# Performance work log

Hardware: AMD Instinct MI355X
Metric: run time of the kernel (lower is better)

Reference implementation:

```python
import jax, jax.numpy as jnp
import numpy as np

D_MODEL = 1024
N_HEADS = 16
HEAD_DIM = D_MODEL // N_HEADS
D_FF = 4096
RANK = 8
B, T = 4, 2048


def _layernorm(x, g, b, eps=1e-5):
    mu = jnp.mean(x, axis=-1, keepdims=True)
    var = jnp.var(x, axis=-1, keepdims=True)
    return (x - mu) * jax.lax.rsqrt(var + eps) * g + b


def _dyn_linear(x, W, A, b_dyn, bias=None):
    # base: x [b,t,i] @ W.T  (W is [o,i] like nn.Linear)
    out = jnp.einsum('bti,oi->bto', x, W)
    if bias is not None:
        out = out + bias
    # per-sample low-rank delta: (x @ b_dyn.T) @ A.T
    delta = jnp.einsum('bti,bri,or->bto', x, b_dyn, A)
    return out + delta


def setup_inputs() -> dict:
    key = jax.random.key(0)
    ks = jax.random.split(key, 24)
    s = 0.02
    inp = {
        'x': jax.random.normal(ks[0], (B, T, D_MODEL), jnp.float32),
        'dyn_q': jax.random.normal(ks[1], (B, RANK, D_MODEL), jnp.float32) * s,
        'dyn_k': jax.random.normal(ks[2], (B, RANK, D_MODEL), jnp.float32) * s,
        'dyn_v': jax.random.normal(ks[3], (B, RANK, D_MODEL), jnp.float32) * s,
        'dyn_ff1': jax.random.normal(ks[4], (B, RANK, D_MODEL), jnp.float32) * s,
        'dyn_ff2': jax.random.normal(ks[5], (B, RANK, D_FF), jnp.float32) * s,
        'Wq': jax.random.normal(ks[6], (D_MODEL, D_MODEL), jnp.float32) / np.sqrt(D_MODEL),
        'Aq': jax.random.normal(ks[7], (D_MODEL, RANK), jnp.float32) * s,
        'Wk': jax.random.normal(ks[8], (D_MODEL, D_MODEL), jnp.float32) / np.sqrt(D_MODEL),
        'Ak': jax.random.normal(ks[9], (D_MODEL, RANK), jnp.float32) * s,
        'Wv': jax.random.normal(ks[10], (D_MODEL, D_MODEL), jnp.float32) / np.sqrt(D_MODEL),
        'Av': jax.random.normal(ks[11], (D_MODEL, RANK), jnp.float32) * s,
        'Wo': jax.random.normal(ks[12], (D_MODEL, D_MODEL), jnp.float32) / np.sqrt(D_MODEL),
        'W1': jax.random.normal(ks[13], (D_FF, D_MODEL), jnp.float32) / np.sqrt(D_MODEL),
        'b1': jnp.zeros((D_FF,), jnp.float32),
        'A1': jax.random.normal(ks[14], (D_FF, RANK), jnp.float32) * s,
        'W2': jax.random.normal(ks[15], (D_MODEL, D_FF), jnp.float32) / np.sqrt(D_FF),
        'b2': jnp.zeros((D_MODEL,), jnp.float32),
        'A2': jax.random.normal(ks[16], (D_MODEL, RANK), jnp.float32) * s,
        'g1': jnp.ones((D_MODEL,), jnp.float32),
        'beta1': jnp.zeros((D_MODEL,), jnp.float32),
        'g2': jnp.ones((D_MODEL,), jnp.float32),
        'beta2': jnp.zeros((D_MODEL,), jnp.float32),
    }
    return inp


def reference(x, dyn_q, dyn_k, dyn_v, dyn_ff1, dyn_ff2,
              Wq, Aq, Wk, Ak, Wv, Av, Wo,
              W1, b1, A1, W2, b2, A2,
              g1, beta1, g2, beta2):
    bsz, seq_len, _ = x.shape
    residual = x
    h = _layernorm(x, g1, beta1)
    q = _dyn_linear(h, Wq, Aq, dyn_q)
    k = _dyn_linear(h, Wk, Ak, dyn_k)
    v = _dyn_linear(h, Wv, Av, dyn_v)
    # [b, t, h, d] -> [b, h, t, d]
    q = q.reshape(bsz, seq_len, N_HEADS, HEAD_DIM).transpose(0, 2, 1, 3)
    k = k.reshape(bsz, seq_len, N_HEADS, HEAD_DIM).transpose(0, 2, 1, 3)
    v = v.reshape(bsz, seq_len, N_HEADS, HEAD_DIM).transpose(0, 2, 1, 3)
    score = jnp.einsum('bhqd,bhkd->bhqk', q, k) / np.sqrt(HEAD_DIM).astype(np.float32)
    attn = jax.nn.softmax(score, axis=-1)
    ctx = jnp.einsum('bhqk,bhkd->bhqd', attn, v)
    ctx = ctx.transpose(0, 2, 1, 3).reshape(bsz, seq_len, D_MODEL)
    x = residual + jnp.einsum('bti,oi->bto', ctx, Wo)  # dropout p=0
    residual = x
    h = _layernorm(x, g2, beta2)
    ff = jax.nn.gelu(_dyn_linear(h, W1, A1, dyn_ff1, bias=b1), approximate=False)
    ff = _dyn_linear(ff, W2, A2, dyn_ff2, bias=b2)
    return residual + ff
```

## Files before the change

### kernel.cpp

```cpp
#include <hip/hip_runtime.h>
#include <math.h>

#define D_MODEL 1024
#define D_FF    4096
#define RANK    8
#define BATCH   4
#define SEQ     2048
#define MTOT    (BATCH*SEQ)
#define NHEADS  16
#define HDIM    64

typedef __attribute__((ext_vector_type(8))) __bf16 bf16x8;
typedef __attribute__((ext_vector_type(4))) float f32x4;
typedef __attribute__((ext_vector_type(8))) unsigned short u16x8;
typedef __attribute__((ext_vector_type(4))) unsigned short u16x4;

__device__ __forceinline__ unsigned short f2bf(float f) {
  __bf16 h = (__bf16)f;
  return __builtin_bit_cast(unsigned short, h);
}
__device__ __forceinline__ float bf2f(unsigned short h) {
  union { unsigned int u; float f; } v; v.u = ((unsigned int)h) << 16;
  return v.f;
}

__device__ __forceinline__ f32x4 mfma16(bf16x8 a, bf16x8 b, f32x4 c) {
  return __builtin_amdgcn_mfma_f32_16x16x32_bf16(a, b, c, 0, 0, 0);
}

#define GLDS(g, l) __builtin_amdgcn_global_load_lds( \
    (const __attribute__((address_space(1))) void*)(g), \
    (__attribute__((address_space(3))) void*)(l), 16, 0, 0)

__global__ __launch_bounds__(256) void cvt_bf16_all(
    const float* __restrict__ s0, const float* __restrict__ s1,
    const float* __restrict__ s2, const float* __restrict__ s3,
    const float* __restrict__ s4, const float* __restrict__ s5,
    unsigned short* __restrict__ d0, unsigned short* __restrict__ d1,
    unsigned short* __restrict__ d2, unsigned short* __restrict__ d3,
    unsigned short* __restrict__ d4, unsigned short* __restrict__ d5)
{
  const int b = blockIdx.x;
  const float* src; unsigned short* dst; int base;
  if (b < 512)       { src = s0; dst = d0; base = b; }
  else if (b < 1024) { src = s1; dst = d1; base = b - 512; }
  else if (b < 1536) { src = s2; dst = d2; base = b - 1024; }
  else if (b < 2048) { src = s3; dst = d3; base = b - 1536; }
  else if (b < 4096) { src = s4; dst = d4; base = b - 2048; }
  else               { src = s5; dst = d5; base = b - 4096; }
  const size_t i = (size_t)base * 256 + threadIdx.x;
  const float4 a  = *reinterpret_cast<const float4*>(src + i * 8);
  const float4 c  = *reinterpret_cast<const float4*>(src + i * 8 + 4);
  u16x8 o;
  o[0] = f2bf(a.x); o[1] = f2bf(a.y); o[2] = f2bf(a.z); o[3] = f2bf(a.w);
  o[4] = f2bf(c.x); o[5] = f2bf(c.y); o[6] = f2bf(c.z); o[7] = f2bf(c.w);
  *reinterpret_cast<u16x8*>(dst + i * 8) = o;
}

__global__ __launch_bounds__(256) void ln_fwd(const float* __restrict__ x,
                                              const float* __restrict__ g,
                                              const float* __restrict__ be,
                                              unsigned short* __restrict__ out)
{
  const int row = blockIdx.x;
  const int t = threadIdx.x;
  const float* xr = x + (size_t)row * D_MODEL;
  float4 vv = *reinterpret_cast<const float4*>(xr + t * 4);
  float s  = vv.x + vv.y + vv.z + vv.w;
  float s2 = vv.x * vv.x + vv.y * vv.y + vv.z * vv.z + vv.w * vv.w;
#pragma unroll
  for (int mm = 1; mm < 64; mm <<= 1) { s += __shfl_xor(s, mm); s2 += __shfl_xor(s2, mm); }
  __shared__ float red[8];
  const int w = t >> 6, l = t & 63;
  if (l == 0) { red[w] = s; red[4 + w] = s2; }
  __syncthreads();
  s  = red[0] + red[1] + red[2] + red[3];
  s2 = red[4] + red[5] + red[6] + red[7];
  float mean = s * (1.f / D_MODEL);
  float var  = s2 * (1.f / D_MODEL) - mean * mean;
  float rstd = rsqrtf(var + 1e-5f);
  float4 gv = *reinterpret_cast<const float4*>(g  + t * 4);
  float4 bv = *reinterpret_cast<const float4*>(be + t * 4);
  u16x4 o;
  o[0] = f2bf((vv.x - mean) * rstd * gv.x + bv.x);
  o[1] = f2bf((vv.y - mean) * rstd * gv.y + bv.y);
  o[2] = f2bf((vv.z - mean) * rstd * gv.z + bv.z);
  o[3] = f2bf((vv.w - mean) * rstd * gv.w + bv.w);
  *reinterpret_cast<u16x4*>(out + (size_t)row * D_MODEL + t * 4) = o;
}

template<int ILEN>
__global__ __launch_bounds__(256) void dyn_u(const unsigned short* __restrict__ hmat,
                                             const float* __restrict__ dyn,
                                             float* __restrict__ u)
{
  const int tid = threadIdx.x, w = tid >> 6, l = tid & 63;
  const int m0 = blockIdx.x * 16 + w * 4;
  const int b = m0 / SEQ;
  const float* dynb = dyn + (size_t)b * RANK * ILEN;
  float acc[4][RANK] = {};
  for (int s = 0; s < ILEN / 64; ++s) {
    const int i = l + s * 64;
    float hv[4];
#pragma unroll
    for (int rr = 0; rr < 4; ++rr) hv[rr] = bf2f(hmat[(size_t)(m0 + rr) * ILEN + i]);
#pragma unroll
    for (int r = 0; r < RANK; ++r) {
      float d = dynb[(size_t)r * ILEN + i];
#pragma unroll
      for (int rr = 0; rr < 4; ++rr) acc[rr][r] += hv[rr] * d;
    }
  }
#pragma unroll
  for (int rr = 0; rr < 4; ++rr)
#pragma unroll
    for (int r = 0; r < RANK; ++r) {
      float a = acc[rr][r];
#pragma unroll
      for (int mm = 1; mm < 64; mm <<= 1) a += __shfl_xor(a, mm);
      if (l == 0) u[(size_t)(m0 + rr) * RANK + r] = a;
    }
}

__global__ __launch_bounds__(256) void dyn_u_qkv(const unsigned short* __restrict__ hmat,
                                                 const float* __restrict__ dq,
                                                 const float* __restrict__ dk,
                                                 const float* __restrict__ dv,
                                                 float* __restrict__ u)
{
  const int tid = threadIdx.x, w = tid >> 6, l = tid & 63;
  const int m0 = blockIdx.x * 16 + w * 4;
  const int b = m0 / SEQ;
  const float* db0 = dq + (size_t)b * RANK * D_MODEL;
  const float* db1 = dk + (size_t)b * RANK * D_MODEL;
  const float* db2 = dv + (size_t)b * RANK * D_MODEL;
  float acc[4][3 * RANK] = {};
  for (int s = 0; s < D_MODEL / 64; ++s) {
    const int i = l + s * 64;
    float hv[4];
#pragma unroll
    for (int rr = 0; rr < 4; ++rr) hv[rr] = bf2f(hmat[(size_t)(m0 + rr) * D_MODEL + i]);
#pragma unroll
    for (int r = 0; r < RANK; ++r) {
      float d0 = db0[(size_t)r * D_MODEL + i];
      float d1 = db1[(size_t)r * D_MODEL + i];
      float d2 = db2[(size_t)r * D_MODEL + i];
#pragma unroll
      for (int rr = 0; rr < 4; ++rr) {
        acc[rr][r] += hv[rr] * d0;
        acc[rr][RANK + r] += hv[rr] * d1;
        acc[rr][2 * RANK + r] += hv[rr] * d2;
      }
    }
  }
#pragma unroll
  for (int g = 0; g < 3; ++g)
#pragma unroll
    for (int rr = 0; rr < 4; ++rr)
#pragma unroll
      for (int r = 0; r < RANK; ++r) {
        float a = acc[rr][g * RANK + r];
#pragma unroll
        for (int mm = 1; mm < 64; mm <<= 1) a += __shfl_xor(a, mm);
        if (l == 0) u[((size_t)g * MTOT + m0 + rr) * RANK + r] = a;
      }
}

template<int NDIM, int KDIM, int MODE, int BN>
__global__ __launch_bounds__(512, (BN == 256) ? 1 : 2)
void gemm_bt(const unsigned short* __restrict__ A,
             const unsigned short* __restrict__ B,
             void* __restrict__ outp,
             void* __restrict__ outp2,
             const float* __restrict__ uvec,
             const float* __restrict__ Ad0,
             const float* __restrict__ Ad1,
             const float* __restrict__ Ad2,
             const float* __restrict__ bias,
             const float* __restrict__ resid)
{
  constexpr bool HAS_DYN = (MODE == 2 || MODE == 3 || MODE == 5);
  constexpr int WN = BN / 64;
  constexpr int WM = 8 / WN;
  constexpr int MSPAN = 256 / WM;
  constexpr int NI = MSPAN / 16;
  __shared__ unsigned short sAB[2][(256 + BN) * 64];
  const int tid = threadIdx.x;
  const int w = tid >> 6, l = tid & 63;

  constexpr int NBX = NDIM / BN;
  constexpr int NWG = NBX * (MTOT / 256);
  const int bid = blockIdx.y * NBX + blockIdx.x;
  const int sbid = (bid & 7) * (NWG / 8) + (bid >> 3);
  const int tm = (sbid / NBX) * 256, tn = (sbid % NBX) * BN;
  const int wm = w / WN, wn = w % WN;

  f32x4 acc[NI][4] = {};

  const int srow = l >> 3;
  const int sc8 = (l & 7) ^ (srow & 7);
  const unsigned short* Ag = A + (size_t)(tm + srow) * KDIM + sc8 * 8;
  const unsigned short* Bg = B + (size_t)(tn + srow) * KDIM + sc8 * 8;

  const int arow = wm * MSPAN + (l & 15);
  const int bcol = wn * 64 + (l & 15);
  const int kb0 = l >> 4;
  const int swz = l & 7;

  constexpr int NT = KDIM / 64;

  auto stage = [&](int buf, int kt) {
    unsigned short* bA = &sAB[buf][0];
    unsigned short* bB = &sAB[buf][256 * 64];
#pragma unroll
    for (int it = 0; it < 4; ++it) {
      const int st = w * 4 + it;
      GLDS(Ag + (size_t)(st * 8) * KDIM + kt, bA + st * 512);
    }
#pragma unroll
    for (int it = 0; it < WN; ++it) {
      const int st = w * WN + it;
      GLDS(Bg + (size_t)(st * 8) * KDIM + kt, bB + st * 512);
    }
  };

  stage(0, 0);
  asm volatile("s_waitcnt vmcnt(0)" ::: "memory");
  __syncthreads();

  int cur = 0;
  for (int t = 0; t < NT; ++t) {
    if (t + 1 < NT) stage(cur ^ 1, (t + 1) * 64);

    const unsigned short* sA_ = &sAB[cur][0];
    const unsigned short* sB_ = &sAB[cur][256 * 64];
#pragma unroll
    for (int kk = 0; kk < 2; ++kk) {
      bf16x8 af[NI], bfv[4];
      const int kphys = ((kk * 4 + kb0) ^ swz) << 3;
#pragma unroll
      for (int i = 0; i < NI; ++i)
        af[i] = *reinterpret_cast<const bf16x8*>(&sA_[(arow + i * 16) * 64 + kphys]);
#pragma unroll
      for (int j = 0; j < 4; ++j)
        bfv[j] = *reinterpret_cast<const bf16x8*>(&sB_[(bcol + j * 16) * 64 + kphys]);
#pragma unroll
      for (int i = 0; i < NI; ++i)
#pragma unroll
        for (int j = 0; j < 4; ++j)
          acc[i][j] = mfma16(af[i], bfv[j], acc[i][j]);
    }
    __syncthreads();
    cur ^= 1;
  }

  const int rbase = tm + wm * MSPAN + ((l >> 4) << 2);
  const int cbase = tn + wn * 64 + (l & 15);

  const int seg = tn >> 10;
  const float* Ad = Ad0;
  const float* uv = uvec;
  if constexpr (MODE == 5) {
    Ad = (seg == 0) ? Ad0 : (seg == 1) ? Ad1 : Ad2;
    uv = uvec + (size_t)seg * ((size_t)MTOT * RANK);
  }

#pragma unroll
  for (int i = 0; i < NI; ++i) {
    float uu[4][8];
    if constexpr (HAS_DYN) {
#pragma unroll
      for (int r = 0; r < 4; ++r) {
        const float* up = uv + (size_t)(rbase + i * 16 + r) * RANK;
#pragma unroll
        for (int p = 0; p < 8; ++p) uu[r][p] = up[p];
      }
    }
#pragma unroll
    for (int j = 0; j < 4; ++j) {
      const int col = cbase + j * 16;
      float ad[8];
      if constexpr (HAS_DYN) {
#pragma unroll
        for (int p = 0; p < 8; ++p) ad[p] = Ad[(size_t)col * RANK + p];
      }
      float vv4[4];
#pragma unroll
      for (int r = 0; r < 4; ++r) {
        const int row = rbase + i * 16 + r;
        float v = acc[i][j][r];
        if constexpr (HAS_DYN) {
#pragma unroll
          for (int p = 0; p < 8; ++p) v += uu[r][p] * ad[p];
        }
        if constexpr (MODE == 2) {
          v += bias[col];
          v = 0.5f * v * (1.f + erff(v * 0.70710678118654752f));
        }
        if constexpr (MODE == 1) {
          v += resid[(size_t)row * NDIM + col];
        }
        if constexpr (MODE == 3) {
          v += bias[col] + resid[(size_t)row * NDIM + col];
        }
        if constexpr (MODE == 5) {
          if (seg == 0) v *= 0.18033688011112042f;
        }
        vv4[r] = v;
      }
      if constexpr (MODE == 2) {
#pragma unroll
        for (int r = 0; r < 4; ++r)
          ((unsigned short*)outp)[(size_t)(rbase + i * 16 + r) * NDIM + col] = f2bf(vv4[r]);
      } else if constexpr (MODE == 5) {
        const int cl = col & 1023;
        if (seg < 2) {
#pragma unroll
          for (int r = 0; r < 4; ++r)
            ((unsigned short*)outp)[((size_t)seg * MTOT + rbase + i * 16 + r) * D_MODEL + cl] =
                f2bf(vv4[r]);
        } else {
          const int row0 = rbase + i * 16;
          const int bb = row0 >> 11, t0 = row0 & (SEQ - 1);
          const int hh = cl >> 6, dd = cl & 63;
          const int jj = (t0 >> 4) & 3;
          unsigned short* vb = &((unsigned short*)outp2)[
              (((size_t)bb * NHEADS + hh) * HDIM + dd) * SEQ + (t0 & ~63)];
#pragma unroll
          for (int dlt = 0; dlt < 4; ++dlt)
            vb[((t0 & 15) + dlt) * 4 + jj] = f2bf(vv4[dlt]);
        }
      } else {
#pragma unroll
        for (int r = 0; r < 4; ++r)
          ((float*)outp)[(size_t)(rbase + i * 16 + r) * NDIM + col] = vv4[r];
      }
    }
  }
}

__global__ __launch_bounds__(256, 4) void attn_fwd(const unsigned short* __restrict__ q,
                                                   const unsigned short* __restrict__ k,
                                                   const unsigned short* __restrict__ vt,
                                                   unsigned short* __restrict__ ctx)
{
  __shared__ unsigned short sK[64 * 64];
  __shared__ unsigned short sV[64 * 64];
  __shared__ unsigned short sP[4][32 * 64];

  const int tid = threadIdx.x, w = tid >> 6, l = tid & 63;
  const int lin = blockIdx.y * (SEQ / 128) + blockIdx.x;
  const int W = (lin & 7) * ((BATCH * NHEADS * SEQ / 128) / 8) + (lin >> 3);
  const int bh = W >> 4, b = bh >> 4, hh = bh & 15;
  const int q0 = (W & 15) * 128 + w * 32;
  const size_t base = ((size_t)b * SEQ) * D_MODEL + hh * HDIM;
  const size_t vtbase = (size_t)bh * HDIM * SEQ;

  bf16x8 qf[2][2];
#pragma unroll
  for (int i = 0; i < 2; ++i)
#pragma unroll
    for (int ks = 0; ks < 2; ++ks)
      qf[i][ks] = *reinterpret_cast<const bf16x8*>(
          &q[base + (size_t)(q0 + i * 16 + (l & 15)) * D_MODEL + ks * 32 + (l >> 4) * 8]);

  bf16x8 ones;
#pragma unroll
  for (int e = 0; e < 8; ++e) ones[e] = (__bf16)1.0f;

  f32x4 oacc[2][4] = {};
  f32x4 sumacc[2] = {};

  const int srow8 = l >> 3;
  const int sswz = (l & 7) ^ (srow8 & 7);
  const unsigned short* kg = k + base + (size_t)srow8 * D_MODEL + sswz * 8;
  const unsigned short* vg = vt + vtbase + (size_t)srow8 * SEQ + sswz * 8;

  const int kb0 = l >> 4;
  const int c15 = l & 15;

  for (int kt = 0; kt < SEQ; kt += 64) {
    __syncthreads();
#pragma unroll
    for (int it = 0; it < 2; ++it) {
      const int c = it * 4 + w;
      GLDS(kg + (size_t)(kt + c * 8) * D_MODEL, sK + c * 512);
      GLDS(vg + (size_t)(c * 8) * SEQ + kt, sV + c * 512);
    }
    asm volatile("s_waitcnt vmcnt(0)" ::: "memory");
    __syncthreads();

    f32x4 sacc[2][4] = {};
    __builtin_amdgcn_s_setprio(1);
#pragma unroll
    for (int ks = 0; ks < 2; ++ks) {
#pragma unroll
      for (int j = 0; j < 4; ++j) {
        const int row = j * 16 + (l & 15);
        bf16x8 kf = *reinterpret_cast<const bf16x8*>(
            &sK[row * 64 + (((ks * 4 + kb0) ^ (row & 7)) << 3)]);
#pragma unroll
        for (int i = 0; i < 2; ++i) sacc[i][j] = mfma16(qf[i][ks], kf, sacc[i][j]);
      }
    }
    __builtin_amdgcn_s_setprio(0);

#pragma unroll
    for (int i = 0; i < 2; ++i) {
#pragma unroll
      for (int r = 0; r < 4; ++r) {
        float p[4];
#pragma unroll
        for (int j = 0; j < 4; ++j) p[j] = __builtin_exp2f(sacc[i][j][r]);
        const int prow = i * 16 + ((l >> 4) << 2) + r;
        u16x4 pk;
        pk[0] = f2bf(p[0]); pk[1] = f2bf(p[1]); pk[2] = f2bf(p[2]); pk[3] = f2bf(p[3]);
        *reinterpret_cast<u16x4*>(
            &sP[w][prow * 64 + ((((c15 >> 1) ^ (prow & 7)) << 3) | ((c15 & 1) << 2))]) = pk;
      }
    }

    __builtin_amdgcn_s_setprio(1);
#pragma unroll
    for (int ks = 0; ks < 2; ++ks) {
      bf16x8 pf[2];
#pragma unroll
      for (int i = 0; i < 2; ++i) {
        const int prw = i * 16 + (l & 15);
        pf[i] = *reinterpret_cast<const bf16x8*>(
            &sP[w][prw * 64 + (((ks * 4 + kb0) ^ (prw & 7)) << 3)]);
      }
#pragma unroll
      for (int j = 0; j < 4; ++j) {
        const int row = j * 16 + (l & 15);
        bf16x8 vf = *reinterpret_cast<const bf16x8*>(
            &sV[row * 64 + (((ks * 4 + kb0) ^ (row & 7)) << 3)]);
#pragma unroll
        for (int i = 0; i < 2; ++i) oacc[i][j] = mfma16(pf[i], vf, oacc[i][j]);
      }
#pragma unroll
      for (int i = 0; i < 2; ++i) sumacc[i] = mfma16(pf[i], ones, sumacc[i]);
    }
    __builtin_amdgcn_s_setprio(0);
  }

#pragma unroll
  for (int i = 0; i < 2; ++i)
#pragma unroll
    for (int r = 0; r < 4; ++r) {
      float inv = 1.f / sumacc[i][r];
      int row = q0 + i * 16 + ((l >> 4) << 2) + r;
#pragma unroll
      for (int j = 0; j < 4; ++j)
        ctx[base + (size_t)row * D_MODEL + j * 16 + (l & 15)] = f2bf(oacc[i][j][r] * inv);
    }
}

extern "C" void kernel_launch(void* const* d_in, const int* in_sizes, int n_in,
                              void* d_out, int out_size, void* d_ws, size_t ws_size,
                              hipStream_t stream)
{
  (void)in_sizes; (void)n_in; (void)out_size; (void)ws_size;
  const float* x      = (const float*)d_in[0];
  const float* dyn_q  = (const float*)d_in[1];
  const float* dyn_k  = (const float*)d_in[2];
  const float* dyn_v  = (const float*)d_in[3];
  const float* dyn_f1 = (const float*)d_in[4];
  const float* dyn_f2 = (const float*)d_in[5];
  const float* Wq = (const float*)d_in[6];
  const float* Aq = (const float*)d_in[7];
  const float* Wk = (const float*)d_in[8];
  const float* Ak = (const float*)d_in[9];
  const float* Wv = (const float*)d_in[10];
  const float* Av = (const float*)d_in[11];
  const float* Wo = (const float*)d_in[12];
  const float* W1 = (const float*)d_in[13];
  const float* b1 = (const float*)d_in[14];
  const float* A1 = (const float*)d_in[15];
  const float* W2 = (const float*)d_in[16];
  const float* b2 = (const float*)d_in[17];
  const float* A2 = (const float*)d_in[18];
  const float* g1 = (const float*)d_in[19];
  const float* be1 = (const float*)d_in[20];
  const float* g2 = (const float*)d_in[21];
  const float* be2 = (const float*)d_in[22];

  char* ws = (char*)d_ws;
  size_t o = 0;
  auto take = [&](size_t b) { size_t r = o; o += (b + 255) & ~(size_t)255; return r; };
  const size_t o_wq = take((size_t)D_MODEL * D_MODEL * 2);
  const size_t o_wk = take((size_t)D_MODEL * D_MODEL * 2);
  const size_t o_wv = take((size_t)D_MODEL * D_MODEL * 2);
  const size_t o_wo = take((size_t)D_MODEL * D_MODEL * 2);
  const size_t o_w1 = take((size_t)D_FF * D_MODEL * 2);
  const size_t o_w2 = take((size_t)D_FF * D_MODEL * 2);
  const size_t o_h1 = take((size_t)MTOT * D_MODEL * 2);
  const size_t o_q  = take((size_t)MTOT * D_MODEL * 2);
  const size_t o_k  = take((size_t)MTOT * D_MODEL * 2);
  const size_t o_v  = take((size_t)MTOT * D_MODEL * 2);
  const size_t o_u  = take((size_t)MTOT * RANK * 4 * 3);
  const size_t o_ff = take((size_t)MTOT * D_FF * 2);

  unsigned short* wq_b = (unsigned short*)(ws + o_wq);
  unsigned short* wk_b = (unsigned short*)(ws + o_wk);
  unsigned short* wv_b = (unsigned short*)(ws + o_wv);
  unsigned short* wo_b = (unsigned short*)(ws + o_wo);
  unsigned short* w1_b = (unsigned short*)(ws + o_w1);
  unsigned short* w2_b = (unsigned short*)(ws + o_w2);
  unsigned short* h1   = (unsigned short*)(ws + o_h1);
  unsigned short* qb   = (unsigned short*)(ws + o_q);
  unsigned short* vtb  = (unsigned short*)(ws + o_v);
  float* u_q  = (float*)(ws + o_u);
  float* u_k  = u_q + (size_t)MTOT * RANK;
  unsigned short* ctx = h1;
  float* x2 = (float*)(ws + o_q);
  unsigned short* h2 = vtb;
  float* u_f1 = u_q;
  float* u_f2 = u_k;
  unsigned short* ffb = (unsigned short*)(ws + o_ff);

  cvt_bf16_all<<<6144, 256, 0, stream>>>(Wq, Wk, Wv, Wo, W1, W2,
                                         wq_b, wk_b, wv_b, wo_b, w1_b, w2_b);

  ln_fwd<<<MTOT, 256, 0, stream>>>(x, g1, be1, h1);

  dyn_u_qkv<<<MTOT / 16, 256, 0, stream>>>(h1, dyn_q, dyn_k, dyn_v, u_q);

  gemm_bt<3 * D_MODEL, D_MODEL, 5, 256><<<dim3(3 * D_MODEL / 256, MTOT / 256), 512, 0, stream>>>(
      h1, wq_b, qb, vtb, u_q, Aq, Ak, Av, nullptr, nullptr);

  attn_fwd<<<dim3(SEQ / 128, BATCH * NHEADS), 256, 0, stream>>>(
      qb, qb + (size_t)MTOT * D_MODEL, vtb, ctx);

  gemm_bt<D_MODEL, D_MODEL, 1, 128><<<dim3(D_MODEL / 128, MTOT / 256), 512, 0, stream>>>(
      ctx, wo_b, x2, nullptr, nullptr, nullptr, nullptr, nullptr, nullptr, x);

  ln_fwd<<<MTOT, 256, 0, stream>>>(x2, g2, be2, h2);

  dyn_u<D_MODEL><<<MTOT / 16, 256, 0, stream>>>(h2, dyn_f1, u_f1);
  gemm_bt<D_FF, D_MODEL, 2, 256><<<dim3(D_FF / 256, MTOT / 256), 512, 0, stream>>>(
      h2, w1_b, ffb, nullptr, u_f1, A1, nullptr, nullptr, b1, nullptr);

  dyn_u<D_FF><<<MTOT / 16, 256, 0, stream>>>(ffb, dyn_f2, u_f2);
  gemm_bt<D_MODEL, D_FF, 3, 128><<<dim3(D_MODEL / 128, MTOT / 256), 512, 0, stream>>>(
      ffb, w2_b, (float*)d_out, nullptr, u_f2, A2, nullptr, nullptr, b2, x2);
}
```

Measured before the change: 540.3 us.

## Fold low-rank dyn delta into GEMM as extra zero-padded K tile

Stores the per-row low-rank projections u and the A adapter matrices as bf16, zero-padded to a 64-wide K slab, and appends that slab as one extra K iteration of the MFMA GEMM main loop. This replaces the scalar 8-term FMA epilogue, with its per-element global loads of u and A, by a single extra matrix-core tile. It adds a small conversion kernel and rounds u and A to bf16, which slightly reduces precision of the delta term.

```diff
diff --git a/kernel.cpp b/kernel.cpp
--- a/kernel.cpp
+++ b/kernel.cpp
@@ -55,6 +55,34 @@
   o[0] = f2bf(a.x); o[1] = f2bf(a.y); o[2] = f2bf(a.z); o[3] = f2bf(a.w);
   o[4] = f2bf(c.x); o[5] = f2bf(c.y); o[6] = f2bf(c.z); o[7] = f2bf(c.w);
   *reinterpret_cast<u16x8*>(dst + i * 8) = o;
+}
+
+__global__ __launch_bounds__(256) void ad_ext(
+    const float* __restrict__ Aq, const float* __restrict__ Ak,
+    const float* __restrict__ Av, const float* __restrict__ A1,
+    const float* __restrict__ A2,
+    unsigned short* __restrict__ eqkv, unsigned short* __restrict__ e1,
+    unsigned short* __restrict__ e2)
+{
+  const int n = blockIdx.x * 256 + threadIdx.x;
+  const float* src; unsigned short* dst;
+  if (n < 3072) {
+    src = (n < 1024) ? (Aq + (size_t)n * 8)
+        : (n < 2048) ? (Ak + (size_t)(n - 1024) * 8)
+                     : (Av + (size_t)(n - 2048) * 8);
+    dst = eqkv + (size_t)n * 64;
+  } else if (n < 7168) {
+    src = A1 + (size_t)(n - 3072) * 8; dst = e1 + (size_t)(n - 3072) * 64;
+  } else {
+    src = A2 + (size_t)(n - 7168) * 8; dst = e2 + (size_t)(n - 7168) * 64;
+  }
+  u16x8 v;
+#pragma unroll
+  for (int p = 0; p < 8; ++p) v[p] = f2bf(src[p]);
+  *reinterpret_cast<u16x8*>(dst) = v;
+  u16x8 z = {};
+#pragma unroll
+  for (int c = 1; c < 8; ++c) *reinterpret_cast<u16x8*>(dst + c * 8) = z;
 }
 
 __global__ __launch_bounds__(256) void ln_fwd(const float* __restrict__ x,
@@ -92,7 +120,7 @@
 template<int ILEN>
 __global__ __launch_bounds__(256) void dyn_u(const unsigned short* __restrict__ hmat,
                                              const float* __restrict__ dyn,
-                                             float* __restrict__ u)
+                                             unsigned short* __restrict__ uext)
 {
   const int tid = threadIdx.x, w = tid >> 6, l = tid & 63;
   const int m0 = blockIdx.x * 16 + w * 4;
@@ -112,21 +140,27 @@
     }
   }
 #pragma unroll
-  for (int rr = 0; rr < 4; ++rr)
+  for (int rr = 0; rr < 4; ++rr) {
+    float red[RANK];
 #pragma unroll
     for (int r = 0; r < RANK; ++r) {
       float a = acc[rr][r];
 #pragma unroll
       for (int mm = 1; mm < 64; mm <<= 1) a += __shfl_xor(a, mm);
-      if (l == 0) u[(size_t)(m0 + rr) * RANK + r] = a;
-    }
+      red[r] = a;
+    }
+    const float mine =
+        (l == 0) ? red[0] : (l == 1) ? red[1] : (l == 2) ? red[2] : (l == 3) ? red[3] :
+        (l == 4) ? red[4] : (l == 5) ? red[5] : (l == 6) ? red[6] : (l == 7) ? red[7] : 0.f;
+    uext[(size_t)(m0 + rr) * 64 + l] = f2bf(mine);
+  }
 }
 
 __global__ __launch_bounds__(256) void dyn_u_qkv(const unsigned short* __restrict__ hmat,
                                                  const float* __restrict__ dq,
                                                  const float* __restrict__ dk,
                                                  const float* __restrict__ dv,
-                                                 float* __restrict__ u)
+                                                 unsigned short* __restrict__ uext)
 {
   const int tid = threadIdx.x, w = tid >> 6, l = tid & 63;
   const int m0 = blockIdx.x * 16 + w * 4;
@@ -156,14 +190,20 @@
 #pragma unroll
   for (int g = 0; g < 3; ++g)
 #pragma unroll
-    for (int rr = 0; rr < 4; ++rr)
+    for (int rr = 0; rr < 4; ++rr) {
+      float red[RANK];
 #pragma unroll
       for (int r = 0; r < RANK; ++r) {
         float a = acc[rr][g * RANK + r];
 #pragma unroll
         for (int mm = 1; mm < 64; mm <<= 1) a += __shfl_xor(a, mm);
-        if (l == 0) u[((size_t)g * MTOT + m0 + rr) * RANK + r] = a;
-      }
+        red[r] = a;
+      }
+      const float mine =
+          (l == 0) ? red[0] : (l == 1) ? red[1] : (l == 2) ? red[2] : (l == 3) ? red[3] :
+          (l == 4) ? red[4] : (l == 5) ? red[5] : (l == 6) ? red[6] : (l == 7) ? red[7] : 0.f;
+      uext[((size_t)g * MTOT + m0 + rr) * 64 + l] = f2bf(mine);
+    }
 }
 
 template<int NDIM, int KDIM, int MODE, int BN>
@@ -172,14 +212,12 @@
              const unsigned short* __restrict__ B,
              void* __restrict__ outp,
              void* __restrict__ outp2,
-             const float* __restrict__ uvec,
-             const float* __restrict__ Ad0,
-             const float* __restrict__ Ad1,
-             const float* __restrict__ Ad2,
+             const unsigned short* __restrict__ Aext,
+             const unsigned short* __restrict__ Bext,
              const float* __restrict__ bias,
              const float* __restrict__ resid)
 {
-  constexpr bool HAS_DYN = (MODE == 2 || MODE == 3 || MODE == 5);
+  constexpr bool HAS_EXT = (MODE == 2 || MODE == 3 || MODE == 5);
   constexpr int WN = BN / 64;
   constexpr int WM = 8 / WN;
   constexpr int MSPAN = 256 / WM;
@@ -194,6 +232,7 @@
   const int sbid = (bid & 7) * (NWG / 8) + (bid >> 3);
   const int tm = (sbid / NBX) * 256, tn = (sbid % NBX) * BN;
   const int wm = w / WN, wn = w % WN;
+  const int seg = tn >> 10;
 
   f32x4 acc[NI][4] = {};
 
@@ -201,6 +240,11 @@
   const int sc8 = (l & 7) ^ (srow & 7);
   const unsigned short* Ag = A + (size_t)(tm + srow) * KDIM + sc8 * 8;
   const unsigned short* Bg = B + (size_t)(tn + srow) * KDIM + sc8 * 8;
+  const size_t aeoff = (MODE == 5) ? (size_t)seg * MTOT : 0;
+  const unsigned short* Ae = HAS_EXT ?
+      (Aext + (aeoff + tm + srow) * 64 + sc8 * 8) : nullptr;
+  const unsigned short* Be = HAS_EXT ?
+      (Bext + (size_t)(tn + srow) * 64 + sc8 * 8) : nullptr;
 
   const int arow = wm * MSPAN + (l & 15);
   const int bcol = wn * 64 + (l & 15);
@@ -208,6 +252,7 @@
   const int swz = l & 7;
 
   constexpr int NT = KDIM / 64;
+  constexpr int TT = HAS_EXT ? NT + 1 : NT;
 
   auto stage = [&](int buf, int kt) {
     unsigned short* bA = &sAB[buf][0];
@@ -223,14 +268,30 @@
       GLDS(Bg + (size_t)(st * 8) * KDIM + kt, bB + st * 512);
     }
   };
+  auto stage_ext = [&](int buf) {
+    unsigned short* bA = &sAB[buf][0];
+    unsigned short* bB = &sAB[buf][256 * 64];
+#pragma unroll
+    for (int it = 0; it < 4; ++it) {
+      const int st = w * 4 + it;
+      GLDS(Ae + (size_t)(st * 8) * 64, bA + st * 512);
+    }
+#pragma unroll
+    for (int it = 0; it < WN; ++it) {
+      const int st = w * WN + it;
+      GLDS(Be + (size_t)(st * 8) * 64, bB + st * 512);
+    }
+  };
 
   stage(0, 0);
   asm volatile("s_waitcnt vmcnt(0)" ::: "memory");
   __syncthreads();
 
   int cur = 0;
-  for (int t = 0; t < NT; ++t) {
-    if (t + 1 < NT) stage(cur ^ 1, (t + 1) * 64);
+  for (int t = 0; t < TT; ++t) {
+    const int nt = t + 1;
+    if (nt < NT) stage(cur ^ 1, nt * 64);
+    else if (HAS_EXT && nt == NT) stage_ext(cur ^ 1);
 
     const unsigned short* sA_ = &sAB[cur][0];
     const unsigned short* sB_ = &sAB[cur][256 * 64];
@@ -257,42 +318,16 @@
   const int rbase = tm + wm * MSPAN + ((l >> 4) << 2);
   const int cbase = tn + wn * 64 + (l & 15);
 
-  const int seg = tn >> 10;
-  const float* Ad = Ad0;
-  const float* uv = uvec;
-  if constexpr (MODE == 5) {
-    Ad = (seg == 0) ? Ad0 : (seg == 1) ? Ad1 : Ad2;
-    uv = uvec + (size_t)seg * ((size_t)MTOT * RANK);
-  }
-
 #pragma unroll
   for (int i = 0; i < NI; ++i) {
-    float uu[4][8];
-    if constexpr (HAS_DYN) {
-#pragma unroll
-      for (int r = 0; r < 4; ++r) {
-        const float* up = uv + (size_t)(rbase + i * 16 + r) * RANK;
-#pragma unroll
-        for (int p = 0; p < 8; ++p) uu[r][p] = up[p];
-      }
-    }
 #pragma unroll
     for (int j = 0; j < 4; ++j) {
       const int col = cbase + j * 16;
-      float ad[8];
-      if constexpr (HAS_DYN) {
-#pragma unroll
-        for (int p = 0; p < 8; ++p) ad[p] = Ad[(size_t)col * RANK + p];
-      }
       float vv4[4];
 #pragma unroll
       for (int r = 0; r < 4; ++r) {
         const int row = rbase + i * 16 + r;
         float v = acc[i][j][r];
-        if constexpr (HAS_DYN) {
-#pragma unroll
-          for (int p = 0; p < 8; ++p) v += uu[r][p] * ad[p];
-        }
         if constexpr (MODE == 2) {
           v += bias[col];
           v = 0.5f * v * (1.f + erff(v * 0.70710678118654752f));
@@ -498,7 +533,10 @@
   const size_t o_q  = take((size_t)MTOT * D_MODEL * 2);
   const size_t o_k  = take((size_t)MTOT * D_MODEL * 2);
   const size_t o_v  = take((size_t)MTOT * D_MODEL * 2);
-  const size_t o_u  = take((size_t)MTOT * RANK * 4 * 3);
+  const size_t o_ue = take((size_t)3 * MTOT * 64 * 2);
+  const size_t o_aq = take((size_t)3 * D_MODEL * 64 * 2);
+  const size_t o_a1 = take((size_t)D_FF * 64 * 2);
+  const size_t o_a2 = take((size_t)D_MODEL * 64 * 2);
   const size_t o_ff = take((size_t)MTOT * D_FF * 2);
 
   unsigned short* wq_b = (unsigned short*)(ws + o_wq);
@@ -510,38 +548,41 @@
   unsigned short* h1   = (unsigned short*)(ws + o_h1);
   unsigned short* qb   = (unsigned short*)(ws + o_q);
   unsigned short* vtb  = (unsigned short*)(ws + o_v);
-  float* u_q  = (float*)(ws + o_u);
-  float* u_k  = u_q + (size_t)MTOT * RANK;
+  unsigned short* ueq  = (unsigned short*)(ws + o_ue);
+  unsigned short* uef1 = ueq;
+  unsigned short* uef2 = ueq + (size_t)MTOT * 64;
+  unsigned short* adeq = (unsigned short*)(ws + o_aq);
+  unsigned short* ade1 = (unsigned short*)(ws + o_a1);
+  unsigned short* ade2 = (unsigned short*)(ws + o_a2);
   unsigned short* ctx = h1;
   float* x2 = (float*)(ws + o_q);
   unsigned short* h2 = vtb;
-  float* u_f1 = u_q;
-  float* u_f2 = u_k;
   unsigned short* ffb = (unsigned short*)(ws + o_ff);
 
   cvt_bf16_all<<<6144, 256, 0, stream>>>(Wq, Wk, Wv, Wo, W1, W2,
                                          wq_b, wk_b, wv_b, wo_b, w1_b, w2_b);
+  ad_ext<<<32, 256, 0, stream>>>(Aq, Ak, Av, A1, A2, adeq, ade1, ade2);
 
   ln_fwd<<<MTOT, 256, 0, stream>>>(x, g1, be1, h1);
 
-  dyn_u_qkv<<<MTOT / 16, 256, 0, stream>>>(h1, dyn_q, dyn_k, dyn_v, u_q);
+  dyn_u_qkv<<<MTOT / 16, 256, 0, stream>>>(h1, dyn_q, dyn_k, dyn_v, ueq);
 
   gemm_bt<3 * D_MODEL, D_MODEL, 5, 256><<<dim3(3 * D_MODEL / 256, MTOT / 256), 512, 0, stream>>>(
-      h1, wq_b, qb, vtb, u_q, Aq, Ak, Av, nullptr, nullptr);
+      h1, wq_b, qb, vtb, ueq, adeq, nullptr, nullptr);
 
   attn_fwd<<<dim3(SEQ / 128, BATCH * NHEADS), 256, 0, stream>>>(
       qb, qb + (size_t)MTOT * D_MODEL, vtb, ctx);
 
   gemm_bt<D_MODEL, D_MODEL, 1, 128><<<dim3(D_MODEL / 128, MTOT / 256), 512, 0, stream>>>(
-      ctx, wo_b, x2, nullptr, nullptr, nullptr, nullptr, nullptr, nullptr, x);
+      ctx, wo_b, x2, nullptr, nullptr, nullptr, nullptr, x);
 
   ln_fwd<<<MTOT, 256, 0, stream>>>(x2, g2, be2, h2);
 
-  dyn_u<D_MODEL><<<MTOT / 16, 256, 0, stream>>>(h2, dyn_f1, u_f1);
+  dyn_u<D_MODEL><<<MTOT / 16, 256, 0, stream>>>(h2, dyn_f1, uef1);
   gemm_bt<D_FF, D_MODEL, 2, 256><<<dim3(D_FF / 256, MTOT / 256), 512, 0, stream>>>(
-      h2, w1_b, ffb, nullptr, u_f1, A1, nullptr, nullptr, b1, nullptr);
-
-  dyn_u<D_FF><<<MTOT / 16, 256, 0, stream>>>(ffb, dyn_f2, u_f2);
+      h2, w1_b, ffb, nullptr, uef1, ade1, b1, nullptr);
+
+  dyn_u<D_FF><<<MTOT / 16, 256, 0, stream>>>(ffb, dyn_f2, uef2);
   gemm_bt<D_MODEL, D_FF, 3, 128><<<dim3(D_MODEL / 128, MTOT / 256), 512, 0, stream>>>(
-      ffb, w2_b, (float*)d_out, nullptr, u_f2, A2, nullptr, nullptr, b2, x2);
-}
+      ffb, w2_b, (float*)d_out, nullptr, uef2, ade2, b2, x2);
+}
```

New measurement: 503.0 us. 1.07x faster.
